# Kernel optimization log

Measured on AMD Instinct MI355X. Metric: run time of the kernel, lower is better.

Reference implementation:

```python
import jax, jax.numpy as jnp
import numpy as np

N = 50000       # num nodes
E = 400000      # num edges (before self loops)
IN, HID, H, OUT = 128, 64, 4, 64
SLOPE = 0.2     # PyG GATv2Conv default negative_slope


def setup_inputs() -> dict:
    key = jax.random.key(0)
    ks = jax.random.split(key, 14)
    def lin(k, fan_in, fan_out):
        return jax.random.normal(k, (fan_in, fan_out), jnp.float32) / np.sqrt(fan_in)
    return {
        "x": jax.random.normal(ks[0], (N, IN), jnp.float32),
        "edge_index": jax.random.randint(ks[1], (2, E), 0, N, jnp.int32),
        # layer 1: in=IN -> HID per head, H heads, concat
        "Wl1": lin(ks[2], IN, H * HID), "bl1": jnp.zeros((H * HID,), jnp.float32),
        "Wr1": lin(ks[3], IN, H * HID), "br1": jnp.zeros((H * HID,), jnp.float32),
        "att1": jax.random.normal(ks[4], (H, HID), jnp.float32) / np.sqrt(HID),
        "bias1": jnp.zeros((H * HID,), jnp.float32),
        # layer 2: in=H*HID -> OUT, 1 head, concat=False
        "Wl2": lin(ks[5], H * HID, OUT), "bl2": jnp.zeros((OUT,), jnp.float32),
        "Wr2": lin(ks[6], H * HID, OUT), "br2": jnp.zeros((OUT,), jnp.float32),
        "att2": jax.random.normal(ks[7], (1, OUT), jnp.float32) / np.sqrt(OUT),
        "bias2": jnp.zeros((OUT,), jnp.float32),
    }


def gatv2_conv(x, src, dst, Wl, bl, Wr, br, att, heads, out_ch, num_nodes):
    """PyG GATv2Conv (share_weights=False). src->dst aggregation at dst."""
    xl = (x @ Wl + bl).reshape(-1, heads, out_ch)  # source transform (x_j)
    xr = (x @ Wr + br).reshape(-1, heads, out_ch)  # target transform (x_i)
    m = xl[src] + xr[dst]                          # [E, H, C]
    e = jnp.sum(jax.nn.leaky_relu(m, SLOPE) * att, axis=-1)  # [E, H]
    # segment softmax over incoming edges of each dst node
    emax = jax.ops.segment_max(e, dst, num_segments=num_nodes)
    ex = jnp.exp(e - emax[dst])
    denom = jax.ops.segment_sum(ex, dst, num_segments=num_nodes)
    alpha = ex / denom[dst]                        # [E, H]
    out = jax.ops.segment_sum(alpha[:, :, None] * xl[src], dst, num_segments=num_nodes)
    return out  # [N, H, C]


def reference(x, edge_index, Wl1, bl1, Wr1, br1, att1, bias1,
              Wl2, bl2, Wr2, br2, att2, bias2):
    n = x.shape[0]
    loops = jnp.arange(n, dtype=edge_index.dtype)
    src = jnp.concatenate([edge_index[0], loops])  # add_self_loops=True
    dst = jnp.concatenate([edge_index[1], loops])
    h = gatv2_conv(x, src, dst, Wl1, bl1, Wr1, br1, att1, H, HID, n)
    h = h.reshape(n, H * HID) + bias1              # concat=True
    h = jax.nn.elu(h)                              # dropout=0.0
    o = gatv2_conv(h, src, dst, Wl2, bl2, Wr2, br2, att2, 1, OUT, n)
    return o.reshape(n, OUT) + bias2               # concat=False, heads=1
```

## Files before the change

### kernel.cpp

```cpp
#include <hip/hip_runtime.h>
#include <hip/hip_bf16.h>

typedef unsigned short u16;
typedef __attribute__((ext_vector_type(8))) short short8;
typedef __attribute__((ext_vector_type(4))) float floatx4;
typedef __attribute__((ext_vector_type(2))) float f32x2;

#define N_NODES 50000
#define N_EDGES 400000
#define ET      450000
#define F_IN    128
#define C1      256
#define HID     64
#define OUTC    64
#define SLOPE   0.2f
#define LIN1_BLOCKS 782
#define LOG2E   1.44269504089f

#if __has_builtin(__builtin_amdgcn_exp2f)
#define EXP2(x) __builtin_amdgcn_exp2f(x)
#else
#define EXP2(x) __expf((x) * 0.69314718056f)
#endif

__device__ __forceinline__ float bf2f(u16 v) {
    return __uint_as_float(((unsigned)v) << 16);
}
__device__ __forceinline__ float bflo(unsigned u) { return __uint_as_float(u << 16); }
__device__ __forceinline__ float bfhi(unsigned u) { return __uint_as_float(u & 0xffff0000u); }
__device__ __forceinline__ u16 f2bf(float f) {
    unsigned u = __float_as_uint(f);
    return (u16)((u + 0x7fffu + ((u >> 16) & 1u)) >> 16);
}
__device__ __forceinline__ f32x2 up2(unsigned u) {
    f32x2 r; r.x = bflo(u); r.y = bfhi(u); return r;
}
template<int CTRL>
__device__ __forceinline__ float dpp_add(float x) {
    return x + __int_as_float(__builtin_amdgcn_update_dpp(
        0, __float_as_int(x), CTRL, 0xF, 0xF, true));
}
__device__ __forceinline__ float red16(float p) {
    p = dpp_add<0xB1>(p);
    p = dpp_add<0x4E>(p);
    p = dpp_add<0x141>(p);
    p = dpp_add<0x140>(p);
    return p;
}
template<int CTRL>
__device__ __forceinline__ f32x2 dpp_add2(f32x2 x) {
    f32x2 o;
    o.x = __int_as_float(__builtin_amdgcn_update_dpp(
        0, __float_as_int(x.x), CTRL, 0xF, 0xF, true));
    o.y = __int_as_float(__builtin_amdgcn_update_dpp(
        0, __float_as_int(x.y), CTRL, 0xF, 0xF, true));
    return x + o;
}
__device__ __forceinline__ f32x2 red16x2(f32x2 p) {
    p = dpp_add2<0xB1>(p);
    p = dpp_add2<0x4E>(p);
    p = dpp_add2<0x141>(p);
    p = dpp_add2<0x140>(p);
    return p;
}
__device__ __forceinline__ bool detect_f32(const unsigned* __restrict__ xw) {
    unsigned w = xw[threadIdx.x & 63];
    unsigned aexp = (w >> 7) & 0xFFu;
    unsigned long long b = __ballot(aexp >= 170u || aexp <= 40u);
    return __popcll(b) >= 16;
}

__global__ __launch_bounds__(256) void convert_all_kernel(
    const unsigned* __restrict__ xw,
    const void* wl1, const void* wr1, const void* wl2, const void* wr2,
    const void* s0, const void* s1, const void* s2, const void* s3,
    const void* s4, const void* s5, const void* s6, const void* s7,
    u16* __restrict__ wt, u16* __restrict__ prm, int* __restrict__ hist)
{
    if (blockIdx.x >= 385) {
        int idx = (blockIdx.x - 385) * 256 + threadIdx.x;
        if (idx < N_NODES) hist[idx] = 0;
        return;
    }
    bool f32m = detect_f32(xw);
    if (blockIdx.x == 384) {
        for (int t = threadIdx.x; t < 1280; t += 256) {
            const void* src; int local;
            if      (t < 256)  { src = s0; local = t; }
            else if (t < 512)  { src = s1; local = t - 256; }
            else if (t < 768)  { src = s2; local = t - 512; }
            else if (t < 1024) { src = s3; local = t - 768; }
            else if (t < 1088) { src = s4; local = t - 1024; }
            else if (t < 1152) { src = s5; local = t - 1088; }
            else if (t < 1216) { src = s6; local = t - 1152; }
            else               { src = s7; local = t - 1216; }
            prm[t] = f32m ? f2bf(((const float*)src)[local]) : ((const u16*)src)[local];
        }
        return;
    }
    int t = blockIdx.x * 256 + threadIdx.x;
    const void* src; int local, k, n, K, base;
    if (t < 32768)      { src = wl1; local = t;         k = local >> 8; n = local & 255; K = 128; base = 0; }
    else if (t < 65536) { src = wr1; local = t - 32768; k = local >> 8; n = local & 255; K = 128; base = 32768; }
    else if (t < 81920) { src = wl2; local = t - 65536; k = local >> 6; n = local & 63;  K = 256; base = 65536; }
    else                { src = wr2; local = t - 81920; k = local >> 6; n = local & 63;  K = 256; base = 81920; }
    u16 v = f32m ? f2bf(((const float*)src)[local]) : ((const u16*)src)[local];
    wt[base + n * K + k] = v;
}

__global__ __launch_bounds__(256) void scan1_kernel(const int* __restrict__ hist,
                                                    int* __restrict__ rowptr,
                                                    int* __restrict__ bsum)
{
    int t = threadIdx.x;
    int i = blockIdx.x * 256 + t;
    int v = (i < N_NODES) ? hist[i] : 0;
    __shared__ int sd[256];
    sd[t] = v;
    __syncthreads();
    #pragma unroll
    for (int ofs = 1; ofs < 256; ofs <<= 1) {
        int u = (t >= ofs) ? sd[t - ofs] : 0;
        __syncthreads();
        sd[t] += u;
        __syncthreads();
    }
    if (i < N_NODES) rowptr[i] = sd[t] - v;
    if (t == 255) bsum[blockIdx.x] = sd[255];
}

__global__ __launch_bounds__(256) void scan3_kernel(int* __restrict__ rowptr,
                                                    const int* __restrict__ bsum,
                                                    int* __restrict__ off)
{
    int t = threadIdx.x;
    int v = (t < (int)blockIdx.x) ? bsum[t] : 0;
    __shared__ int sd[256];
    sd[t] = v;
    __syncthreads();
    #pragma unroll
    for (int ofs = 1; ofs < 256; ofs <<= 1) {
        int u = (t >= ofs) ? sd[t - ofs] : 0;
        __syncthreads();
        sd[t] += u;
        __syncthreads();
    }
    int boff = sd[255];
    int i = blockIdx.x * 256 + t;
    if (i < N_NODES) {
        int r = rowptr[i] + boff;
        rowptr[i] = r;
        off[i] = r;
    }
}

__global__ __launch_bounds__(256) void scatter_kernel(const int* __restrict__ ei,
                                                      int* __restrict__ off,
                                                      int* __restrict__ src_csr)
{
    int t = blockIdx.x * 256 + threadIdx.x;
    if (t >= ET) return;
    int s, d;
    if (t < N_EDGES) { s = ei[t]; d = ei[N_EDGES + t]; } else { s = d = t - N_EDGES; }
    int pos = atomicAdd(&off[d], 1);
    src_csr[pos] = s;
}

__global__ __launch_bounds__(256) void lin1_hist_kernel(
    const u16* __restrict__ X, const u16* __restrict__ Wt,
    const u16* __restrict__ bl, const u16* __restrict__ br,
    u16* __restrict__ Yl, u16* __restrict__ Yr, int nrows,
    const int* __restrict__ ei, int* __restrict__ hist)
{
    constexpr int K = 128, N = 256, LS = K + 8;
    __shared__ __align__(16) u16 sX[64 * LS];
    __shared__ __align__(16) u16 sW[64 * LS];

    if (blockIdx.x >= LIN1_BLOCKS) {
        int t = (blockIdx.x - LIN1_BLOCKS) * 256 + threadIdx.x;
        if (t < ET) {
            int d = (t < N_EDGES) ? ei[N_EDGES + t] : t - N_EDGES;
            atomicAdd(&hist[d], 1);
        }
        return;
    }

    const bool f32m = detect_f32((const unsigned*)X);
    const float* X32 = (const float*)X;
    const int row0 = blockIdx.x * 64;
    const int wave = threadIdx.x >> 6, lane = threadIdx.x & 63;
    const int quad = lane >> 4, l16 = lane & 15;

    for (int i = threadIdx.x * 8; i < 64 * K; i += 2048) {
        int r = i >> 7, c = i & 127;
        int gr = row0 + r;
        u16* dst = &sX[r * LS + c];
        if (f32m) {
            float4 v0 = make_float4(0.f, 0.f, 0.f, 0.f), v1 = v0;
            if (gr < nrows) {
                v0 = *(const float4*)&X32[(size_t)gr * K + c];
                v1 = *(const float4*)&X32[(size_t)gr * K + c + 4];
            }
            ushort4 p0, p1;
            p0.x = f2bf(v0.x); p0.y = f2bf(v0.y); p0.z = f2bf(v0.z); p0.w = f2bf(v0.w);
            p1.x = f2bf(v1.x); p1.y = f2bf(v1.y); p1.z = f2bf(v1.z); p1.w = f2bf(v1.w);
            *(ushort4*)dst = p0;
            *(ushort4*)(dst + 4) = p1;
        } else {
            uint4 v = {0u, 0u, 0u, 0u};
            if (gr < nrows) v = *(const uint4*)&X[(size_t)gr * K + c];
            *(uint4*)dst = v;
        }
    }
    __syncthreads();

    short8 a[4];
    #pragma unroll
    for (int kk = 0; kk < 4; ++kk)
        a[kk] = *(const short8*)&sX[(wave * 16 + l16) * LS + kk * 32 + quad * 8];

    for (int side = 0; side < 2; ++side) {
        const u16* wbase = Wt + side * (N * K);
        const u16* bias  = side ? br : bl;
        u16* Y = side ? Yr : Yl;
        for (int ch = 0; ch < 4; ++ch) {
            __syncthreads();
            for (int i = threadIdx.x * 8; i < 64 * K; i += 2048) {
                int n = i >> 7, c = i & 127;
                *(uint4*)&sW[n * LS + c] = *(const uint4*)&wbase[(size_t)(ch * 64 + n) * K + c];
            }
            __syncthreads();
            floatx4 acc0 = {0.f, 0.f, 0.f, 0.f}, acc1 = acc0, acc2 = acc0, acc3 = acc0;
            #pragma unroll
            for (int kk = 0; kk < 4; ++kk) {
                short8 b0 = *(const short8*)&sW[(l16) * LS + kk * 32 + quad * 8];
                short8 b1 = *(const short8*)&sW[(16 + l16) * LS + kk * 32 + quad * 8];
                short8 b2 = *(const short8*)&sW[(32 + l16) * LS + kk * 32 + quad * 8];
                short8 b3 = *(const short8*)&sW[(48 + l16) * LS + kk * 32 + quad * 8];
                acc0 = __builtin_amdgcn_mfma_f32_16x16x32_bf16(a[kk], b0, acc0, 0, 0, 0);
                acc1 = __builtin_amdgcn_mfma_f32_16x16x32_bf16(a[kk], b1, acc1, 0, 0, 0);
                acc2 = __builtin_amdgcn_mfma_f32_16x16x32_bf16(a[kk], b2, acc2, 0, 0, 0);
                acc3 = __builtin_amdgcn_mfma_f32_16x16x32_bf16(a[kk], b3, acc3, 0, 0, 0);
            }
            const int rbase = row0 + wave * 16 + quad * 4;
            #pragma unroll
            for (int cf = 0; cf < 4; ++cf) {
                const floatx4 av = (cf == 0) ? acc0 : (cf == 1) ? acc1 : (cf == 2) ? acc2 : acc3;
                const int col = ch * 64 + cf * 16 + l16;
                const float bv = bf2f(bias[col]);
                #pragma unroll
                for (int r = 0; r < 4; ++r) {
                    int row = rbase + r;
                    if (row < nrows) Y[(size_t)row * N + col] = f2bf(av[r] + bv);
                }
            }
        }
    }
}

__global__ __launch_bounds__(256) void lin2_fused_kernel(
    const u16* __restrict__ X, const u16* __restrict__ Wt,
    const u16* __restrict__ bl, const u16* __restrict__ br,
    u16* __restrict__ Yl, u16* __restrict__ Yr, int nrows)
{
    constexpr int K = 256, N = 64, LS = K + 8;
    __shared__ __align__(16) u16 sX[64 * LS];
    __shared__ __align__(16) u16 sW[64 * LS];
    const int row0 = blockIdx.x * 64;
    const int wave = threadIdx.x >> 6, lane = threadIdx.x & 63;
    const int quad = lane >> 4, l16 = lane & 15;

    for (int i = threadIdx.x * 8; i < 64 * K; i += 2048) {
        int r = i >> 8, c = i & 255;
        int gr = row0 + r;
        uint4 v = {0u, 0u, 0u, 0u};
        if (gr < nrows) v = *(const uint4*)&X[(size_t)gr * K + c];
        *(uint4*)&sX[r * LS + c] = v;
    }
    __syncthreads();

    short8 a[8];
    #pragma unroll
    for (int kk = 0; kk < 8; ++kk)
        a[kk] = *(const short8*)&sX[(wave * 16 + l16) * LS + kk * 32 + quad * 8];

    for (int side = 0; side < 2; ++side) {
        const u16* wbase = Wt + side * (N * K);
        const u16* bias  = side ? br : bl;
        u16* Y = side ? Yr : Yl;
        __syncthreads();
        for (int i = threadIdx.x * 8; i < 64 * K; i += 2048) {
            int n = i >> 8, c = i & 255;
            *(uint4*)&sW[n * LS + c] = *(const uint4*)&wbase[(size_t)n * K + c];
        }
        __syncthreads();
        floatx4 acc0 = {0.f, 0.f, 0.f, 0.f}, acc1 = acc0, acc2 = acc0, acc3 = acc0;
        #pragma unroll
        for (int kk = 0; kk < 8; ++kk) {
            short8 b0 = *(const short8*)&sW[(l16) * LS + kk * 32 + quad * 8];
            short8 b1 = *(const short8*)&sW[(16 + l16) * LS + kk * 32 + quad * 8];
            short8 b2 = *(const short8*)&sW[(32 + l16) * LS + kk * 32 + quad * 8];
            short8 b3 = *(const short8*)&sW[(48 + l16) * LS + kk * 32 + quad * 8];
            acc0 = __builtin_amdgcn_mfma_f32_16x16x32_bf16(a[kk], b0, acc0, 0, 0, 0);
            acc1 = __builtin_amdgcn_mfma_f32_16x16x32_bf16(a[kk], b1, acc1, 0, 0, 0);
            acc2 = __builtin_amdgcn_mfma_f32_16x16x32_bf16(a[kk], b2, acc2, 0, 0, 0);
            acc3 = __builtin_amdgcn_mfma_f32_16x16x32_bf16(a[kk], b3, acc3, 0, 0, 0);
        }
        const int rbase = row0 + wave * 16 + quad * 4;
        #pragma unroll
        for (int cf = 0; cf < 4; ++cf) {
            const floatx4 av = (cf == 0) ? acc0 : (cf == 1) ? acc1 : (cf == 2) ? acc2 : acc3;
            const int col = cf * 16 + l16;
            const float bv = bf2f(bias[col]);
            #pragma unroll
            for (int r = 0; r < 4; ++r) {
                int row = rbase + r;
                if (row < nrows) Y[(size_t)row * N + col] = f2bf(av[r] + bv);
            }
        }
    }
}

__global__ __launch_bounds__(64, 6) void node1_kernel(
    const u16* __restrict__ xl, const u16* __restrict__ xr,
    const int* __restrict__ rowptr, const int* __restrict__ hist,
    const int* __restrict__ src_csr, const u16* __restrict__ att,
    const u16* __restrict__ bias, u16* __restrict__ hout)
{
    const int d = blockIdx.x;
    const int l = threadIdx.x;
    const int start = __builtin_amdgcn_readfirstlane(rowptr[d]);
    const int deg = __builtin_amdgcn_readfirstlane(hist[d]);
    const int dm1 = deg - 1;
    const u16* __restrict__ xlp = xl + l * 4;

    uint2 auv = *(const uint2*)&att[l * 4];
    const f32x2 atA = up2(auv.x) * LOG2E, atB = up2(auv.y) * LOG2E;
    uint2 ruv = *(const uint2*)&xr[(size_t)d * C1 + l * 4];
    const f32x2 rA = up2(ruv.x), rB = up2(ruv.y);

    float m = -1e30f, la = 0.f;
    f32x2 accA = {0.f, 0.f}, accB = {0.f, 0.f};

    int s0 = __builtin_amdgcn_readfirstlane(src_csr[start]);
    int s1 = __builtin_amdgcn_readfirstlane(src_csr[start + min(1, dm1)]);
    int s2 = __builtin_amdgcn_readfirstlane(src_csr[start + min(2, dm1)]);
    int s3 = __builtin_amdgcn_readfirstlane(src_csr[start + min(3, dm1)]);
    uint2 u0 = *(const uint2*)&xlp[(size_t)s0 * C1];
    uint2 u1 = *(const uint2*)&xlp[(size_t)s1 * C1];
    uint2 u2 = *(const uint2*)&xlp[(size_t)s2 * C1];
    uint2 u3 = *(const uint2*)&xlp[(size_t)s3 * C1];

    int j = 0;
    for (; j + 4 <= deg; j += 4) {
        const uint2 c0 = u0, c1 = u1, c2 = u2, c3 = u3;
        const int jn = j + 4;
        if (jn < deg) {
            int t0 = __builtin_amdgcn_readfirstlane(src_csr[start + jn]);
            int t1 = __builtin_amdgcn_readfirstlane(src_csr[start + min(jn + 1, dm1)]);
            int t2 = __builtin_amdgcn_readfirstlane(src_csr[start + min(jn + 2, dm1)]);
            int t3 = __builtin_amdgcn_readfirstlane(src_csr[start + min(jn + 3, dm1)]);
            u0 = *(const uint2*)&xlp[(size_t)t0 * C1];
            u1 = *(const uint2*)&xlp[(size_t)t1 * C1];
            u2 = *(const uint2*)&xlp[(size_t)t2 * C1];
            u3 = *(const uint2*)&xlp[(size_t)t3 * C1];
        }
        f32x2 x0A = up2(c0.x), x0B = up2(c0.y);
        f32x2 x1A = up2(c1.x), x1B = up2(c1.y);
        f32x2 x2A = up2(c2.x), x2B = up2(c2.y);
        f32x2 x3A = up2(c3.x), x3B = up2(c3.y);
        f32x2 t, pv;
        t = x0A + rA; t = __builtin_elementwise_max(t, t * SLOPE); pv  = t * atA;
        t = x0B + rB; t = __builtin_elementwise_max(t, t * SLOPE); pv += t * atB;
        float p0 = pv.x + pv.y;
        t = x1A + rA; t = __builtin_elementwise_max(t, t * SLOPE); pv  = t * atA;
        t = x1B + rB; t = __builtin_elementwise_max(t, t * SLOPE); pv += t * atB;
        float p1 = pv.x + pv.y;
        t = x2A + rA; t = __builtin_elementwise_max(t, t * SLOPE); pv  = t * atA;
        t = x2B + rB; t = __builtin_elementwise_max(t, t * SLOPE); pv += t * atB;
        float p2 = pv.x + pv.y;
        t = x3A + rA; t = __builtin_elementwise_max(t, t * SLOPE); pv  = t * atA;
        t = x3B + rB; t = __builtin_elementwise_max(t, t * SLOPE); pv += t * atB;
        float p3 = pv.x + pv.y;
        f32x2 P01 = {p0, p1}, P23 = {p2, p3};
        P01 = red16x2(P01);
        P23 = red16x2(P23);
        p0 = P01.x; p1 = P01.y; p2 = P23.x; p3 = P23.y;
        float pm = fmaxf(fmaxf(p0, p1), fmaxf(p2, p3));
        if (__any(pm > m)) {
            float mn = fmaxf(m, pm);
            float sc = EXP2(m - mn);
            la *= sc; accA *= sc; accB *= sc;
            m = mn;
        }
        float w0 = EXP2(p0 - m);
        float w1 = EXP2(p1 - m);
        float w2 = EXP2(p2 - m);
        float w3 = EXP2(p3 - m);
        la += w0 + w1 + w2 + w3;
        accA += x0A * w0 + x1A * w1 + x2A * w2 + x3A * w3;
        accB += x0B * w0 + x1B * w1 + x2B * w2 + x3B * w3;
    }
    if (j < deg) {
        const bool v1 = j + 1 < deg, v2 = j + 2 < deg;
        f32x2 x0A = up2(u0.x), x0B = up2(u0.y);
        f32x2 x1A = up2(u1.x), x1B = up2(u1.y);
        f32x2 x2A = up2(u2.x), x2B = up2(u2.y);
        f32x2 t, pv;
        t = x0A + rA; t = __builtin_elementwise_max(t, t * SLOPE); pv  = t * atA;
        t = x0B + rB; t = __builtin_elementwise_max(t, t * SLOPE); pv += t * atB;
        float p0 = pv.x + pv.y;
        t = x1A + rA; t = __builtin_elementwise_max(t, t * SLOPE); pv  = t * atA;
        t = x1B + rB; t = __builtin_elementwise_max(t, t * SLOPE); pv += t * atB;
        float p1 = pv.x + pv.y;
        t = x2A + rA; t = __builtin_elementwise_max(t, t * SLOPE); pv  = t * atA;
        t = x2B + rB; t = __builtin_elementwise_max(t, t * SLOPE); pv += t * atB;
        float p2 = pv.x + pv.y;
        f32x2 P01 = {p0, p1};
        P01 = red16x2(P01);
        p0 = P01.x; p1 = P01.y;
        p2 = red16(p2);
        float pm = p0;
        if (v1) pm = fmaxf(pm, p1);
        if (v2) pm = fmaxf(pm, p2);
        if (__any(pm > m)) {
            float mn = fmaxf(m, pm);
            float sc = EXP2(m - mn);
            la *= sc; accA *= sc; accB *= sc;
            m = mn;
        }
        float w0 = EXP2(p0 - m);
        float w1 = v1 ? EXP2(p1 - m) : 0.f;
        float w2 = v2 ? EXP2(p2 - m) : 0.f;
        la += w0 + w1 + w2;
        accA += x0A * w0 + x1A * w1 + x2A * w2;
        accB += x0B * w0 + x1B * w1 + x2B * w2;
    }
    const float inv = 1.f / la;
    const int c = l * 4;
    float v0 = accA.x * inv + bf2f(bias[c + 0]);
    float v1 = accA.y * inv + bf2f(bias[c + 1]);
    float v2 = accB.x * inv + bf2f(bias[c + 2]);
    float v3 = accB.y * inv + bf2f(bias[c + 3]);
    v0 = v0 > 0.f ? v0 : __expf(fminf(v0, 0.f)) - 1.f;
    v1 = v1 > 0.f ? v1 : __expf(fminf(v1, 0.f)) - 1.f;
    v2 = v2 > 0.f ? v2 : __expf(fminf(v2, 0.f)) - 1.f;
    v3 = v3 > 0.f ? v3 : __expf(fminf(v3, 0.f)) - 1.f;
    ushort4 o;
    o.x = f2bf(v0); o.y = f2bf(v1); o.z = f2bf(v2); o.w = f2bf(v3);
    *(ushort4*)&hout[(size_t)d * C1 + c] = o;
}

__global__ __launch_bounds__(64, 8) void node2_kernel(
    const u16* __restrict__ xl, const u16* __restrict__ xr,
    const int* __restrict__ rowptr, const int* __restrict__ hist,
    const int* __restrict__ src_csr, const u16* __restrict__ att,
    const u16* __restrict__ bias, void* __restrict__ outp,
    const unsigned* __restrict__ xorig)
{
    const bool f32o = detect_f32(xorig);
    const int d = blockIdx.x;
    const int l = threadIdx.x;
    const int start = __builtin_amdgcn_readfirstlane(rowptr[d]);
    const int deg = __builtin_amdgcn_readfirstlane(hist[d]);
    const int dm1 = deg - 1;
    const int g = l >> 4, sub = l & 15;
    const int c0 = sub * 4;
    const u16* __restrict__ xlp = xl + c0;

    uint2 auv = *(const uint2*)&att[c0];
    const f32x2 atA = up2(auv.x) * LOG2E, atB = up2(auv.y) * LOG2E;
    uint2 ruv = *(const uint2*)&xr[(size_t)d * OUTC + c0];
    const f32x2 rA = up2(ruv.x), rB = up2(ruv.y);

    float m = -1e30f, la = 0.f;
    f32x2 accA = {0.f, 0.f}, accB = {0.f, 0.f};

    int sA0 = src_csr[start + min(g, dm1)];
    int sA1 = src_csr[start + min(g + 4, dm1)];
    uint2 uA0 = *(const uint2*)&xlp[(size_t)sA0 * OUTC];
    uint2 uA1 = *(const uint2*)&xlp[(size_t)sA1 * OUTC];
    int sB0 = src_csr[start + min(g + 8, dm1)];
    int sB1 = src_csr[start + min(g + 12, dm1)];
    uint2 uB0 = *(const uint2*)&xlp[(size_t)sB0 * OUTC];
    uint2 uB1 = *(const uint2*)&xlp[(size_t)sB1 * OUTC];

    for (int j = 0; j < deg; j += 8) {
        const bool val0 = j + g < deg, val1 = j + g + 4 < deg;
        const uint2 e0 = uA0, e1 = uA1;
        uA0 = uB0; uA1 = uB1;
        if (j + 8 < deg) {
            int t0 = src_csr[start + min(j + 16 + g, dm1)];
            int t1 = src_csr[start + min(j + 20 + g, dm1)];
            uB0 = *(const uint2*)&xlp[(size_t)t0 * OUTC];
            uB1 = *(const uint2*)&xlp[(size_t)t1 * OUTC];
        }
        f32x2 x0A = up2(e0.x), x0B = up2(e0.y);
        f32x2 x1A = up2(e1.x), x1B = up2(e1.y);
        f32x2 t, pv;
        t = x0A + rA; t = __builtin_elementwise_max(t, t * SLOPE); pv  = t * atA;
        t = x0B + rB; t = __builtin_elementwise_max(t, t * SLOPE); pv += t * atB;
        float p0 = pv.x + pv.y;
        t = x1A + rA; t = __builtin_elementwise_max(t, t * SLOPE); pv  = t * atA;
        t = x1B + rB; t = __builtin_elementwise_max(t, t * SLOPE); pv += t * atB;
        float p1 = pv.x + pv.y;
        f32x2 P = {p0, p1};
        P = red16x2(P);
        p0 = P.x; p1 = P.y;
        float q0 = val0 ? p0 : -1e30f;
        float q1 = val1 ? p1 : -1e30f;
        float pm = fmaxf(q0, q1);
        if (__any(pm > m)) {
            float mn = fmaxf(m, pm);
            float sc = EXP2(m - mn);
            la *= sc; accA *= sc; accB *= sc;
            m = mn;
        }
        float w0 = val0 ? EXP2(p0 - m) : 0.f;
        float w1 = val1 ? EXP2(p1 - m) : 0.f;
        la += w0 + w1;
        accA += x0A * w0 + x1A * w1;
        accB += x0B * w0 + x1B * w1;
    }
    #pragma unroll
    for (int ofs = 16; ofs <= 32; ofs <<= 1) {
        float mo = __shfl_xor(m, ofs);
        float lo = __shfl_xor(la, ofs);
        float bax = __shfl_xor(accA.x, ofs);
        float bay = __shfl_xor(accA.y, ofs);
        float bbx = __shfl_xor(accB.x, ofs);
        float bby = __shfl_xor(accB.y, ofs);
        float mn = fmaxf(m, mo);
        float e0 = EXP2(m - mn), e1 = EXP2(mo - mn);
        la = la * e0 + lo * e1;
        accA.x = accA.x * e0 + bax * e1;
        accA.y = accA.y * e0 + bay * e1;
        accB.x = accB.x * e0 + bbx * e1;
        accB.y = accB.y * e0 + bby * e1;
        m = mn;
    }
    if (g == 0) {
        const float inv = 1.f / la;
        float v0 = accA.x * inv + bf2f(bias[c0 + 0]);
        float v1 = accA.y * inv + bf2f(bias[c0 + 1]);
        float v2 = accB.x * inv + bf2f(bias[c0 + 2]);
        float v3 = accB.y * inv + bf2f(bias[c0 + 3]);
        if (f32o) {
            float4 o = make_float4(v0, v1, v2, v3);
            *(float4*)&((float*)outp)[(size_t)d * OUTC + c0] = o;
        } else {
            ushort4 o;
            o.x = f2bf(v0); o.y = f2bf(v1); o.z = f2bf(v2); o.w = f2bf(v3);
            *(ushort4*)&((u16*)outp)[(size_t)d * OUTC + c0] = o;
        }
    }
}

extern "C" void kernel_launch(void* const* d_in, const int* in_sizes, int n_in,
                              void* d_out, int out_size, void* d_ws, size_t ws_size,
                              hipStream_t stream)
{
    const void* x  = d_in[0];
    const int*  ei = (const int*)d_in[1];

    char* ws = (char*)d_ws;
    u16* xl1     = (u16*)(ws + 0);
    u16* xr1     = (u16*)(ws + 25600000);
    u16* hbuf    = (u16*)(ws + 51200000);
    u16* xl2     = (u16*)(ws + 0);
    u16* xr2     = (u16*)(ws + 6400000);
    int* hist    = (int*)(ws + 76800000);
    int* rowptr  = (int*)(ws + 77000000);
    int* off     = (int*)(ws + 77200000);
    int* src_csr = (int*)(ws + 77400000);
    u16* prm     = (u16*)(ws + 79200064);
    u16* wt      = (u16*)(ws + 79210240);
    int* bsum    = (int*)(ws + 79410000);

    u16* bl1   = prm + 0;
    u16* br1   = prm + 256;
    u16* att1  = prm + 512;
    u16* bias1 = prm + 768;
    u16* bl2   = prm + 1024;
    u16* br2   = prm + 1088;
    u16* att2  = prm + 1152;
    u16* bias2 = prm + 1216;
    u16* wt1   = wt + 0;
    u16* wt2   = wt + 65536;

    convert_all_kernel<<<581, 256, 0, stream>>>(
        (const unsigned*)x,
        d_in[2], d_in[4], d_in[8], d_in[10],
        d_in[3], d_in[5], d_in[6], d_in[7], d_in[9], d_in[11], d_in[12], d_in[13],
        wt, prm, hist);

    const int eb = (ET + 255) / 256;
    lin1_hist_kernel<<<LIN1_BLOCKS + eb, 256, 0, stream>>>(
        (const u16*)x, wt1, bl1, br1, xl1, xr1, N_NODES, ei, hist);

    scan1_kernel<<<196, 256, 0, stream>>>(hist, rowptr, bsum);
    scan3_kernel<<<196, 256, 0, stream>>>(rowptr, bsum, off);
    scatter_kernel<<<eb, 256, 0, stream>>>(ei, off, src_csr);

    node1_kernel<<<N_NODES, 64, 0, stream>>>(xl1, xr1, rowptr, hist, src_csr, att1, bias1, hbuf);
    lin2_fused_kernel<<<(N_NODES + 63) / 64, 256, 0, stream>>>(hbuf, wt2, bl2, br2, xl2, xr2, N_NODES);
    node2_kernel<<<N_NODES, 64, 0, stream>>>(xl2, xr2, rowptr, hist, src_csr, att2, bias2, d_out,
                                             (const unsigned*)x);
}
```

Baseline: 240.4 us.

## Prepack weights in MFMA fragment order and load B operands directly from global

The weight-transpose prep kernel now writes weights in a per-lane MFMA fragment layout, so each lane can fetch its short8 B operand with one contiguous 16-byte load. Both linear kernels drop the shared-memory weight tile and its __syncthreads barriers and read B fragments straight from global memory, which should be L2-resident. This removes the LDS staging round-trip and block-wide barriers per chunk, and cuts LDS use, which may allow more blocks per CU. In exchange there is more global/L2 load traffic per wave and higher register pressure from holding 16 B fragments.

```diff
diff --git a/kernel.cpp b/kernel.cpp
--- a/kernel.cpp
+++ b/kernel.cpp
@@ -99,13 +99,30 @@
         return;
     }
     int t = blockIdx.x * 256 + threadIdx.x;
-    const void* src; int local, k, n, K, base;
-    if (t < 32768)      { src = wl1; local = t;         k = local >> 8; n = local & 255; K = 128; base = 0; }
-    else if (t < 65536) { src = wr1; local = t - 32768; k = local >> 8; n = local & 255; K = 128; base = 32768; }
-    else if (t < 81920) { src = wl2; local = t - 65536; k = local >> 6; n = local & 63;  K = 256; base = 65536; }
-    else                { src = wr2; local = t - 81920; k = local >> 6; n = local & 63;  K = 256; base = 81920; }
+    const void* src; int local, k, n, dst;
+    if (t < 32768) {
+        src = wl1; local = t; k = local >> 8; n = local & 255;
+        int ch = n >> 6, cf = (n >> 4) & 3, l16 = n & 15;
+        int kk = k >> 5, quad = (k >> 3) & 3, j = k & 7;
+        dst = 0 + ((ch * 4 + cf) * 4 + kk) * 512 + (quad * 16 + l16) * 8 + j;
+    } else if (t < 65536) {
+        src = wr1; local = t - 32768; k = local >> 8; n = local & 255;
+        int ch = n >> 6, cf = (n >> 4) & 3, l16 = n & 15;
+        int kk = k >> 5, quad = (k >> 3) & 3, j = k & 7;
+        dst = 32768 + ((ch * 4 + cf) * 4 + kk) * 512 + (quad * 16 + l16) * 8 + j;
+    } else if (t < 81920) {
+        src = wl2; local = t - 65536; k = local >> 6; n = local & 63;
+        int cf = n >> 4, l16 = n & 15;
+        int kk = k >> 5, quad = (k >> 3) & 3, j = k & 7;
+        dst = 65536 + (cf * 8 + kk) * 512 + (quad * 16 + l16) * 8 + j;
+    } else {
+        src = wr2; local = t - 81920; k = local >> 6; n = local & 63;
+        int cf = n >> 4, l16 = n & 15;
+        int kk = k >> 5, quad = (k >> 3) & 3, j = k & 7;
+        dst = 81920 + (cf * 8 + kk) * 512 + (quad * 16 + l16) * 8 + j;
+    }
     u16 v = f32m ? f2bf(((const float*)src)[local]) : ((const u16*)src)[local];
-    wt[base + n * K + k] = v;
+    wt[dst] = v;
 }
 
 __global__ __launch_bounds__(256) void scan1_kernel(const int* __restrict__ hist,
@@ -167,14 +184,13 @@
 }
 
 __global__ __launch_bounds__(256) void lin1_hist_kernel(
-    const u16* __restrict__ X, const u16* __restrict__ Wt,
+    const u16* __restrict__ X, const u16* __restrict__ Wp,
     const u16* __restrict__ bl, const u16* __restrict__ br,
     u16* __restrict__ Yl, u16* __restrict__ Yr, int nrows,
     const int* __restrict__ ei, int* __restrict__ hist)
 {
     constexpr int K = 128, N = 256, LS = K + 8;
     __shared__ __align__(16) u16 sX[64 * LS];
-    __shared__ __align__(16) u16 sW[64 * LS];
 
     if (blockIdx.x >= LIN1_BLOCKS) {
         int t = (blockIdx.x - LIN1_BLOCKS) * 256 + threadIdx.x;
@@ -219,28 +235,26 @@
     for (int kk = 0; kk < 4; ++kk)
         a[kk] = *(const short8*)&sX[(wave * 16 + l16) * LS + kk * 32 + quad * 8];
 
+    const u16* wlane = Wp + lane * 8;
     for (int side = 0; side < 2; ++side) {
-        const u16* wbase = Wt + side * (N * K);
         const u16* bias  = side ? br : bl;
         u16* Y = side ? Yr : Yl;
+        const u16* wside = wlane + side * 32768;
         for (int ch = 0; ch < 4; ++ch) {
-            __syncthreads();
-            for (int i = threadIdx.x * 8; i < 64 * K; i += 2048) {
-                int n = i >> 7, c = i & 127;
-                *(uint4*)&sW[n * LS + c] = *(const uint4*)&wbase[(size_t)(ch * 64 + n) * K + c];
-            }
-            __syncthreads();
+            const u16* wch = wside + ch * 8192;
+            short8 b[16];
+            #pragma unroll
+            for (int cf = 0; cf < 4; ++cf)
+                #pragma unroll
+                for (int kk = 0; kk < 4; ++kk)
+                    b[cf * 4 + kk] = *(const short8*)&wch[(cf * 4 + kk) * 512];
             floatx4 acc0 = {0.f, 0.f, 0.f, 0.f}, acc1 = acc0, acc2 = acc0, acc3 = acc0;
             #pragma unroll
             for (int kk = 0; kk < 4; ++kk) {
-                short8 b0 = *(const short8*)&sW[(l16) * LS + kk * 32 + quad * 8];
-                short8 b1 = *(const short8*)&sW[(16 + l16) * LS + kk * 32 + quad * 8];
-                short8 b2 = *(const short8*)&sW[(32 + l16) * LS + kk * 32 + quad * 8];
-                short8 b3 = *(const short8*)&sW[(48 + l16) * LS + kk * 32 + quad * 8];
-                acc0 = __builtin_amdgcn_mfma_f32_16x16x32_bf16(a[kk], b0, acc0, 0, 0, 0);
-                acc1 = __builtin_amdgcn_mfma_f32_16x16x32_bf16(a[kk], b1, acc1, 0, 0, 0);
-                acc2 = __builtin_amdgcn_mfma_f32_16x16x32_bf16(a[kk], b2, acc2, 0, 0, 0);
-                acc3 = __builtin_amdgcn_mfma_f32_16x16x32_bf16(a[kk], b3, acc3, 0, 0, 0);
+                acc0 = __builtin_amdgcn_mfma_f32_16x16x32_bf16(a[kk], b[kk],      acc0, 0, 0, 0);
+                acc1 = __builtin_amdgcn_mfma_f32_16x16x32_bf16(a[kk], b[4 + kk],  acc1, 0, 0, 0);
+                acc2 = __builtin_amdgcn_mfma_f32_16x16x32_bf16(a[kk], b[8 + kk],  acc2, 0, 0, 0);
+                acc3 = __builtin_amdgcn_mfma_f32_16x16x32_bf16(a[kk], b[12 + kk], acc3, 0, 0, 0);
             }
             const int rbase = row0 + wave * 16 + quad * 4;
             #pragma unroll
@@ -259,13 +273,12 @@
 }
 
 __global__ __launch_bounds__(256) void lin2_fused_kernel(
-    const u16* __restrict__ X, const u16* __restrict__ Wt,
+    const u16* __restrict__ X, const u16* __restrict__ Wp,
     const u16* __restrict__ bl, const u16* __restrict__ br,
     u16* __restrict__ Yl, u16* __restrict__ Yr, int nrows)
 {
     constexpr int K = 256, N = 64, LS = K + 8;
     __shared__ __align__(16) u16 sX[64 * LS];
-    __shared__ __align__(16) u16 sW[64 * LS];
     const int row0 = blockIdx.x * 64;
     const int wave = threadIdx.x >> 6, lane = threadIdx.x & 63;
     const int quad = lane >> 4, l16 = lane & 15;
@@ -284,38 +297,28 @@
     for (int kk = 0; kk < 8; ++kk)
         a[kk] = *(const short8*)&sX[(wave * 16 + l16) * LS + kk * 32 + quad * 8];
 
+    const u16* wlane = Wp + lane * 8;
     for (int side = 0; side < 2; ++side) {
-        const u16* wbase = Wt + side * (N * K);
         const u16* bias  = side ? br : bl;
         u16* Y = side ? Yr : Yl;
-        __syncthreads();
-        for (int i = threadIdx.x * 8; i < 64 * K; i += 2048) {
-            int n = i >> 8, c = i & 255;
-            *(uint4*)&sW[n * LS + c] = *(const uint4*)&wbase[(size_t)n * K + c];
-        }
-        __syncthreads();
-        floatx4 acc0 = {0.f, 0.f, 0.f, 0.f}, acc1 = acc0, acc2 = acc0, acc3 = acc0;
-        #pragma unroll
-        for (int kk = 0; kk < 8; ++kk) {
-            short8 b0 = *(const short8*)&sW[(l16) * LS + kk * 32 + quad * 8];
-            short8 b1 = *(const short8*)&sW[(16 + l16) * LS + kk * 32 + quad * 8];
-            short8 b2 = *(const short8*)&sW[(32 + l16) * LS + kk * 32 + quad * 8];
-            short8 b3 = *(const short8*)&sW[(48 + l16) * LS + kk * 32 + quad * 8];
-            acc0 = __builtin_amdgcn_mfma_f32_16x16x32_bf16(a[kk], b0, acc0, 0, 0, 0);
-            acc1 = __builtin_amdgcn_mfma_f32_16x16x32_bf16(a[kk], b1, acc1, 0, 0, 0);
-            acc2 = __builtin_amdgcn_mfma_f32_16x16x32_bf16(a[kk], b2, acc2, 0, 0, 0);
-            acc3 = __builtin_amdgcn_mfma_f32_16x16x32_bf16(a[kk], b3, acc3, 0, 0, 0);
-        }
-        const int rbase = row0 + wave * 16 + quad * 4;
+        const u16* wside = wlane + side * 16384;
         #pragma unroll
         for (int cf = 0; cf < 4; ++cf) {
-            const floatx4 av = (cf == 0) ? acc0 : (cf == 1) ? acc1 : (cf == 2) ? acc2 : acc3;
+            short8 b[8];
+            #pragma unroll
+            for (int kk = 0; kk < 8; ++kk)
+                b[kk] = *(const short8*)&wside[(cf * 8 + kk) * 512];
+            floatx4 acc = {0.f, 0.f, 0.f, 0.f};
+            #pragma unroll
+            for (int kk = 0; kk < 8; ++kk)
+                acc = __builtin_amdgcn_mfma_f32_16x16x32_bf16(a[kk], b[kk], acc, 0, 0, 0);
+            const int rbase = row0 + wave * 16 + quad * 4;
             const int col = cf * 16 + l16;
             const float bv = bf2f(bias[col]);
             #pragma unroll
             for (int r = 0; r < 4; ++r) {
                 int row = rbase + r;
-                if (row < nrows) Y[(size_t)row * N + col] = f2bf(av[r] + bv);
+                if (row < nrows) Y[(size_t)row * N + col] = f2bf(acc[r] + bv);
             }
         }
     }
```

New measurement: 241.3 us. No clear change (+0.4%).
